# Kernel tuning notes

Measured on AMD Instinct MI355X. Metric: run time of the kernel, lower is better.

Reference implementation:

```python
import jax, jax.numpy as jnp
import numpy as np

DIM = 1024
CROSS_DIM = 768
NUM_HEADS = 16
HEAD_DIM = DIM // NUM_HEADS
B, S, SC = 4, 2048, 1024


def setup_inputs() -> dict:
    key = jax.random.key(0)
    ks = jax.random.split(key, 12)
    x = jax.random.normal(ks[0], (B, S, DIM), dtype=jnp.float32)
    cross_x = jax.random.normal(ks[1], (B, SC, CROSS_DIM), dtype=jnp.float32)
    # ragged cross lengths -> padding mask (True = ignore)
    lengths = jax.random.randint(ks[2], (B,), SC // 2, SC + 1)
    key_padding_mask = jnp.arange(SC)[None, :] >= lengths[:, None]  # (B, SC) bool
    s = 0.02
    Wq = jax.random.normal(ks[3], (DIM, DIM), dtype=jnp.float32) * s
    bq = jnp.zeros((DIM,), dtype=jnp.float32)
    Wk = jax.random.normal(ks[4], (CROSS_DIM, DIM), dtype=jnp.float32) * s
    bk = jnp.zeros((DIM,), dtype=jnp.float32)
    Wv = jax.random.normal(ks[5], (CROSS_DIM, DIM), dtype=jnp.float32) * s
    bv = jnp.zeros((DIM,), dtype=jnp.float32)
    Wo = jax.random.normal(ks[6], (DIM, DIM), dtype=jnp.float32) * s
    bo = jnp.zeros((DIM,), dtype=jnp.float32)
    return {"x": x, "cross_x": cross_x, "key_padding_mask": key_padding_mask,
            "Wq": Wq, "bq": bq, "Wk": Wk, "bk": bk, "Wv": Wv, "bv": bv,
            "Wo": Wo, "bo": bo}


def reference(x, cross_x, key_padding_mask, Wq, bq, Wk, bk, Wv, bv, Wo, bo):
    b, s, _ = x.shape
    sc = cross_x.shape[1]
    # projections (torch Linear: x @ W + b with W stored as (in, out) here)
    q = (x @ Wq + bq).reshape(b, s, NUM_HEADS, HEAD_DIM).transpose(0, 2, 1, 3)
    k = (cross_x @ Wk + bk).reshape(b, sc, NUM_HEADS, HEAD_DIM).transpose(0, 2, 1, 3)
    v = (cross_x @ Wv + bv).reshape(b, sc, NUM_HEADS, HEAD_DIM).transpose(0, 2, 1, 3)
    # (b, h, s, sc) attention scores
    scores = jnp.einsum('bhsd,bhcd->bhsc', q, k) / jnp.sqrt(jnp.float32(HEAD_DIM))
    mask = key_padding_mask[:, None, None, :]  # (b,1,1,sc), True = ignore
    scores = jnp.where(mask, -jnp.inf, scores)
    # original subtracts row max then softmax; equivalent stable softmax
    scores = scores - jnp.max(scores, axis=-1, keepdims=True)
    attn = jax.nn.softmax(scores, axis=-1)
    out = jnp.einsum('bhsc,bhcd->bhsd', attn, v)
    out = out.transpose(0, 2, 1, 3).reshape(b, s, DIM)
    return out @ Wo + bo
```

## Files before the change

### kernel.cpp

```cpp
#include <hip/hip_runtime.h>
#include <hip/hip_bf16.h>
#include <stdint.h>

#define DIM_ 1024
#define NH_ 16
#define HD_ 64
#define B_ 4
#define S_ 2048
#define SC_ 1024
#define CD_ 768

typedef __attribute__((ext_vector_type(8))) short bf16x8;
typedef __attribute__((ext_vector_type(4))) short bf16x4;
typedef __attribute__((ext_vector_type(4))) float f32x4;

__device__ inline unsigned short f2bf(float f) {
    __hip_bfloat16 h = __float2bfloat16(f);
    return __builtin_bit_cast(unsigned short, h);
}

__device__ inline f32x4 vmax4(f32x4 a, f32x4 b) {
    f32x4 r;
#pragma unroll
    for (int i = 0; i < 4; ++i) r[i] = fmaxf(a[i], b[i]);
    return r;
}

#define GLOAD16(SRC, DST) __builtin_amdgcn_global_load_lds( \
    (const __attribute__((address_space(1))) void*)(SRC),   \
    (__attribute__((address_space(3))) void*)(DST), 16, 0, 0)

__global__ void k_f32_to_bf16(const float* __restrict__ in, unsigned short* __restrict__ out, int n4) {
    int i = blockIdx.x * blockDim.x + threadIdx.x;
    int stride = gridDim.x * blockDim.x;
    for (; i < n4; i += stride) {
        float4 v = ((const float4*)in)[i];
        uint2 pk;
        pk.x = (unsigned int)f2bf(v.x) | ((unsigned int)f2bf(v.y) << 16);
        pk.y = (unsigned int)f2bf(v.z) | ((unsigned int)f2bf(v.w) << 16);
        ((uint2*)out)[i] = pk;
    }
}

__global__ void k_transposeW4(const float* __restrict__ Wq, const float* __restrict__ Wk,
                              const float* __restrict__ Wv, const float* __restrict__ Wo,
                              unsigned short* __restrict__ WQT, unsigned short* __restrict__ WKT,
                              unsigned short* __restrict__ WVT, unsigned short* __restrict__ WOT) {
    int idx = blockIdx.x * blockDim.x + threadIdx.x;
    const float* W; unsigned short* WT; int K;
    if (idx < 131072)      { W = Wq; WT = WQT; K = 1024; }
    else if (idx < 229376) { W = Wk; WT = WKT; K = 768;  idx -= 131072; }
    else if (idx < 327680) { W = Wv; WT = WVT; K = 768;  idx -= 229376; }
    else                   { W = Wo; WT = WOT; K = 1024; idx -= 327680; }
    int n = idx & 1023;
    int k0 = (idx >> 10) << 3;
    unsigned int pk[4];
#pragma unroll
    for (int j = 0; j < 4; ++j) {
        unsigned short a = f2bf(W[(size_t)(k0 + 2 * j) * 1024 + n]);
        unsigned short b = f2bf(W[(size_t)(k0 + 2 * j + 1) * 1024 + n]);
        pk[j] = (unsigned int)a | ((unsigned int)b << 16);
    }
    *(uint4*)&WT[(size_t)n * K + k0] = *(uint4*)pk;
}

__global__ void k_mask_bits(const unsigned int* __restrict__ m,
                            unsigned int* __restrict__ bits, int* __restrict__ ntp) {
    __shared__ int bm_s;
    __shared__ unsigned int wbits[128];
    if (threadIdx.x == 0) bm_s = 0;
    __syncthreads();
    int any = 0;
    for (int i = threadIdx.x; i < 1024; i += 256)
        if (m[i] > 1u) any = 1;
    if (any) atomicOr(&bm_s, 1);
    __syncthreads();
    const int boolmode = bm_s;
    const int w = threadIdx.x;
    if (w < 128) {
        const unsigned char* mb = (const unsigned char*)m;
        unsigned int out = 0;
        for (int j = 0; j < 32; ++j) {
            int c = w * 32 + j;
            int masked = boolmode ? (mb[c] != 0) : (m[c] != 0u);
            out |= (unsigned int)masked << j;
        }
        bits[w] = out;
        wbits[w] = out;
    }
    __syncthreads();
    if (threadIdx.x < 4) {
        int nt = 0;
        for (int tt = 0; tt < 16; ++tt) {
            unsigned int w0 = wbits[threadIdx.x * 32 + tt * 2];
            unsigned int w1 = wbits[threadIdx.x * 32 + tt * 2 + 1];
            if ((w0 & w1) != 0xFFFFFFFFu) nt = tt + 1;
        }
        ntp[threadIdx.x] = nt;
    }
}

template<int EPI>
__global__ __launch_bounds__(256) void k_gemm_bt(
    const unsigned short* __restrict__ A, const unsigned short* __restrict__ BT,
    const float* __restrict__ bias, const float* __restrict__ bias2, float oscale,
    unsigned short* __restrict__ Cb, unsigned short* __restrict__ Cb2,
    float* __restrict__ Cf, int M, int N, int K)
{
    __shared__ unsigned short As[2][128 * 32];
    __shared__ unsigned short Bs[2][128 * 32];
    const int t = threadIdx.x;
    const int w = t >> 6, lane = t & 63;
    const int lo = lane & 15, hi = lane >> 4;
    const int nwg = gridDim.x * gridDim.y;
    const int wg = blockIdx.y * gridDim.x + blockIdx.x;
    const int swz = (wg & 7) * (nwg >> 3) + (wg >> 3);
    const int m0 = (swz % gridDim.x) * 128, n0 = (swz / gridDim.x) * 128;
    const int wr = (w >> 1) * 64, wc = (w & 1) * 64;
    const int srow = lane >> 2;
    const int scol = (lane & 3) * 8;

    f32x4 zero4 = {0.f, 0.f, 0.f, 0.f};
    f32x4 acc[4][4];
    for (int i = 0; i < 4; ++i)
        for (int j = 0; j < 4; ++j) acc[i][j] = zero4;

#pragma unroll
    for (int p = 0; p < 2; ++p) {
        int chunk = w * 2 + p;
        int r = chunk * 16 + srow;
        GLOAD16(&A[(size_t)(m0 + r) * K + scol], &As[0][chunk * 512]);
        GLOAD16(&BT[(size_t)(n0 + r) * K + scol], &Bs[0][chunk * 512]);
    }
    __syncthreads();

    int cur = 0;
    for (int k0 = 0; k0 < K; k0 += 32) {
        if (k0 + 32 < K) {
#pragma unroll
            for (int p = 0; p < 2; ++p) {
                int chunk = w * 2 + p;
                int r = chunk * 16 + srow;
                GLOAD16(&A[(size_t)(m0 + r) * K + k0 + 32 + scol], &As[cur ^ 1][chunk * 512]);
                GLOAD16(&BT[(size_t)(n0 + r) * K + k0 + 32 + scol], &Bs[cur ^ 1][chunk * 512]);
            }
        }
        bf16x8 af[4], bfr[4];
#pragma unroll
        for (int i = 0; i < 4; ++i)
            af[i] = *(const bf16x8*)&As[cur][(wr + i * 16 + lo) * 32 + (hi << 3)];
#pragma unroll
        for (int j = 0; j < 4; ++j)
            bfr[j] = *(const bf16x8*)&Bs[cur][(wc + j * 16 + lo) * 32 + (hi << 3)];
#pragma unroll
        for (int i = 0; i < 4; ++i)
#pragma unroll
            for (int j = 0; j < 4; ++j)
                acc[i][j] = __builtin_amdgcn_mfma_f32_16x16x32_bf16(af[i], bfr[j], acc[i][j], 0, 0, 0);
        __syncthreads();
        cur ^= 1;
    }

#pragma unroll
    for (int i = 0; i < 4; ++i) {
#pragma unroll
        for (int j = 0; j < 4; ++j) {
            int n = n0 + wc + j * 16 + lo;
            int mbase = m0 + wr + i * 16 + (hi << 2);
            if (EPI == 3 && n >= 1024) {
                float b2 = bias2[n - 1024];
                uint2 pk;
                pk.x = (unsigned int)f2bf(acc[i][j][0] + b2) | ((unsigned int)f2bf(acc[i][j][1] + b2) << 16);
                pk.y = (unsigned int)f2bf(acc[i][j][2] + b2) | ((unsigned int)f2bf(acc[i][j][3] + b2) << 16);
                int bb = mbase >> 10, c = mbase & 1023;
                *(uint2*)&Cb2[(size_t)((bb << 10) + (n - 1024)) * 1024 + c] = pk;
            } else {
#pragma unroll
                for (int r = 0; r < 4; ++r) {
                    int m = mbase + r;
                    if (EPI == 0) {
                        float v = (acc[i][j][r] + bias[n]) * oscale;
                        Cb[(size_t)m * 1024 + n] = f2bf(v);
                    } else if (EPI == 2) {
                        float v = (acc[i][j][r] + bias[n]) * oscale;
                        Cf[(size_t)m * 1024 + n] = v;
                    } else {
                        float v = acc[i][j][r] + bias[n];
                        Cb[(size_t)m * 1024 + n] = f2bf(v);
                    }
                }
            }
        }
    }
}

__global__ __launch_bounds__(256) void k_attn(
    const unsigned short* __restrict__ Q, const unsigned short* __restrict__ Kb,
    const unsigned short* __restrict__ VT, const unsigned int* __restrict__ bits,
    const int* __restrict__ ntp, unsigned short* __restrict__ Ob)
{
    __shared__ unsigned short lds[16384];
    const int t = threadIdx.x, w = t >> 6, lane = t & 63;
    const int lo = lane & 15, hi = lane >> 4;
    const int qt = blockIdx.x, h = blockIdx.y, b = blockIdx.z;
    const int qr0 = qt * 128 + w * 32;
    const int l7 = lo & 7;
    const int nt = ntp[b];

    const int srow = lane >> 3;
    const int scb  = ((lane & 7) ^ srow) << 3;

    bf16x8 qf[2][2];
#pragma unroll
    for (int qh = 0; qh < 2; ++qh)
#pragma unroll
        for (int kk = 0; kk < 2; ++kk)
            qf[qh][kk] = *(const bf16x8*)&Q[(size_t)(b * S_ + qr0 + qh * 16 + lo) * DIM_ + h * 64 + kk * 32 + hi * 8];

    f32x4 zero4 = {0.f, 0.f, 0.f, 0.f};
    float mrow[2] = {-1e30f, -1e30f}, lsum[2] = {0.f, 0.f};
    f32x4 o[4][2];
#pragma unroll
    for (int dt = 0; dt < 4; ++dt)
#pragma unroll
        for (int qh = 0; qh < 2; ++qh) o[dt][qh] = zero4;

#pragma unroll
    for (int s = 0; s < 2; ++s) {
        int rl = w * 16 + s * 8 + srow;
        GLOAD16(&Kb[(size_t)(b * SC_ + rl) * DIM_ + h * 64 + scb], &lds[(w * 16 + s * 8) * 64]);
        GLOAD16(&VT[(size_t)(b * 1024 + h * 64 + rl) * SC_ + scb], &lds[8192 + (w * 16 + s * 8) * 64]);
    }
    __syncthreads();

    int cur = 0;
    for (int tt = 0; tt < nt; ++tt) {
        if (tt + 1 < nt) {
            int c0n = (tt + 1) * 64;
#pragma unroll
            for (int s = 0; s < 2; ++s) {
                int rl = w * 16 + s * 8 + srow;
                GLOAD16(&Kb[(size_t)(b * SC_ + c0n + rl) * DIM_ + h * 64 + scb],
                        &lds[(cur ^ 1) * 4096 + (w * 16 + s * 8) * 64]);
                GLOAD16(&VT[(size_t)(b * 1024 + h * 64 + rl) * SC_ + c0n + scb],
                        &lds[8192 + (cur ^ 1) * 4096 + (w * 16 + s * 8) * 64]);
            }
        }
        const unsigned short* Kl = &lds[cur * 4096];
        const unsigned short* Vl = &lds[8192 + cur * 4096];

        f32x4 st[4][2];
#pragma unroll
        for (int n = 0; n < 4; ++n)
#pragma unroll
            for (int qh = 0; qh < 2; ++qh) st[n][qh] = zero4;
#pragma unroll
        for (int n = 0; n < 4; ++n) {
            const int R = n * 16 + lo;
            bf16x8 k0 = *(const bf16x8*)&Kl[R * 64 + ((hi ^ l7) << 3)];
            bf16x8 k1 = *(const bf16x8*)&Kl[R * 64 + (((4 + hi) ^ l7) << 3)];
#pragma unroll
            for (int qh = 0; qh < 2; ++qh) {
                st[n][qh] = __builtin_amdgcn_mfma_f32_16x16x32_bf16(k0, qf[qh][0], st[n][qh], 0, 0, 0);
                st[n][qh] = __builtin_amdgcn_mfma_f32_16x16x32_bf16(k1, qf[qh][1], st[n][qh], 0, 0, 0);
            }
        }
        bf16x4 vf[4][4];
#pragma unroll
        for (int dt = 0; dt < 4; ++dt)
#pragma unroll
            for (int n = 0; n < 4; ++n)
                vf[dt][n] = *(const bf16x4*)&Vl[(dt * 16 + lo) * 64
                              + (((2 * n + (hi >> 1)) ^ l7) << 3) + ((hi & 1) << 2)];

        uint2 mw = *(const uint2*)&bits[b * 32 + tt * 2];

        f32x4 p[2][4];
        float mx[2];
        if ((mw.x | mw.y) == 0u) {
#pragma unroll
            for (int qh = 0; qh < 2; ++qh) {
                f32x4 a = vmax4(vmax4(st[0][qh], st[1][qh]), vmax4(st[2][qh], st[3][qh]));
                mx[qh] = fmaxf(fmaxf(a[0], a[1]), fmaxf(a[2], a[3]));
#pragma unroll
                for (int n = 0; n < 4; ++n) p[qh][n] = st[n][qh];
            }
        } else {
            mx[0] = -1e30f; mx[1] = -1e30f;
#pragma unroll
            for (int n = 0; n < 4; ++n) {
                unsigned int wd = (n & 2) ? mw.y : mw.x;
#pragma unroll
                for (int r = 0; r < 4; ++r) {
                    int sh = ((n & 1) << 4) + (hi << 2) + r;
                    bool mk = (wd >> sh) & 1u;
#pragma unroll
                    for (int qh = 0; qh < 2; ++qh) {
                        float s = mk ? -1e30f : st[n][qh][r];
                        p[qh][n][r] = s;
                        mx[qh] = fmaxf(mx[qh], s);
                    }
                }
            }
        }
        float m2[2];
#pragma unroll
        for (int qh = 0; qh < 2; ++qh) {
            float v = fmaxf(mx[qh], __shfl_xor(mx[qh], 16));
            m2[qh] = fmaxf(v, __shfl_xor(v, 32));
        }
        float growth = fmaxf(m2[0] - mrow[0], m2[1] - mrow[1]);
        if (!__all(growth <= 8.0f)) {
#pragma unroll
            for (int qh = 0; qh < 2; ++qh) {
                float mnew = fmaxf(mrow[qh], m2[qh]);
                float scl = __builtin_amdgcn_exp2f(mrow[qh] - mnew);
                mrow[qh] = mnew;
                lsum[qh] *= scl;
#pragma unroll
                for (int dt = 0; dt < 4; ++dt)
                    o[dt][qh] *= scl;
            }
        }
#pragma unroll
        for (int qh = 0; qh < 2; ++qh) {
            f32x4 rs4 = zero4;
#pragma unroll
            for (int n = 0; n < 4; ++n) {
                f32x4 e;
#pragma unroll
                for (int r = 0; r < 4; ++r)
                    e[r] = __builtin_amdgcn_exp2f(p[qh][n][r] - mrow[qh]);
                p[qh][n] = e;
                rs4 += e;
            }
            float rs = (rs4[0] + rs4[1]) + (rs4[2] + rs4[3]);
            rs += __shfl_xor(rs, 16);
            rs += __shfl_xor(rs, 32);
            lsum[qh] += rs;
        }
#pragma unroll
        for (int qh = 0; qh < 2; ++qh) {
#pragma unroll
            for (int n = 0; n < 4; ++n) {
                uint2 pk2;
                pk2.x = (unsigned int)f2bf(p[qh][n][0]) | ((unsigned int)f2bf(p[qh][n][1]) << 16);
                pk2.y = (unsigned int)f2bf(p[qh][n][2]) | ((unsigned int)f2bf(p[qh][n][3]) << 16);
                bf16x4 pb = __builtin_bit_cast(bf16x4, pk2);
#pragma unroll
                for (int dt = 0; dt < 4; ++dt)
                    o[dt][qh] = __builtin_amdgcn_mfma_f32_16x16x16bf16_1k(vf[dt][n], pb, o[dt][qh], 0, 0, 0);
            }
        }
        __syncthreads();
        cur ^= 1;
    }

    unsigned short* Tl = &lds[w * 2304];
    float inv[2] = {1.0f / lsum[0], 1.0f / lsum[1]};
#pragma unroll
    for (int qh = 0; qh < 2; ++qh)
#pragma unroll
        for (int dt = 0; dt < 4; ++dt)
#pragma unroll
            for (int r = 0; r < 4; ++r)
                Tl[(qh * 16 + lo) * 72 + dt * 16 + hi * 4 + r] = f2bf(o[dt][qh][r] * inv[qh]);
#pragma unroll
    for (int ps = 0; ps < 4; ++ps) {
        int row = ps * 8 + (lane >> 3);
        int col = (lane & 7) * 8;
        bf16x8 v = *(const bf16x8*)&Tl[row * 72 + col];
        *(bf16x8*)&Ob[(size_t)(b * S_ + qr0 + row) * DIM_ + h * 64 + col] = v;
    }
}

extern "C" void kernel_launch(void* const* d_in, const int* in_sizes, int n_in,
                              void* d_out, int out_size, void* d_ws, size_t ws_size,
                              hipStream_t stream)
{
    const float* x  = (const float*)d_in[0];
    const float* cx = (const float*)d_in[1];
    const void* mask = d_in[2];
    const float* Wq = (const float*)d_in[3];
    const float* bq = (const float*)d_in[4];
    const float* Wk = (const float*)d_in[5];
    const float* bk = (const float*)d_in[6];
    const float* Wv = (const float*)d_in[7];
    const float* bv = (const float*)d_in[8];
    const float* Wo = (const float*)d_in[9];
    const float* bo = (const float*)d_in[10];

    unsigned short* ws = (unsigned short*)d_ws;
    const size_t XB  = 0;
    const size_t CXB = XB  + (size_t)8192 * 1024;
    const size_t WQT = CXB + (size_t)4096 * 768;
    const size_t WKT = WQT + (size_t)1024 * 1024;
    const size_t WVT = WKT + (size_t)1024 * 768;
    const size_t WOT = WVT + (size_t)1024 * 768;
    const size_t QB  = WOT + (size_t)1024 * 1024;
    const size_t KB  = QB  + (size_t)8192 * 1024;
    const size_t VTB = KB  + (size_t)4096 * 1024;
    const size_t MBT = VTB + (size_t)4 * 1024 * 1024;
    const size_t NTP = MBT + 256;

    k_f32_to_bf16<<<2048, 256, 0, stream>>>(x,  ws + XB,  8192 * 1024 / 4);
    k_f32_to_bf16<<<2048, 256, 0, stream>>>(cx, ws + CXB, 4096 * 768 / 4);
    k_transposeW4<<<1792, 256, 0, stream>>>(Wq, Wk, Wv, Wo, ws + WQT, ws + WKT, ws + WVT, ws + WOT);
    unsigned int* mbits = (unsigned int*)(ws + MBT);
    int* ntp = (int*)(ws + NTP);
    k_mask_bits<<<1, 256, 0, stream>>>((const unsigned int*)mask, mbits, ntp);

    const float QSCALE = 0.125f * 1.44269504088896340736f;
    dim3 gq(8192 / 128, 1024 / 128);
    dim3 gkv(4096 / 128, 2048 / 128);
    k_gemm_bt<0><<<gq, 256, 0, stream>>>(ws + XB, ws + WQT, bq, nullptr, QSCALE, ws + QB, nullptr, nullptr, 8192, 1024, 1024);
    k_gemm_bt<3><<<gkv, 256, 0, stream>>>(ws + CXB, ws + WKT, bk, bv, 1.0f, ws + KB, ws + VTB, nullptr, 4096, 2048, 768);

    dim3 ga(S_ / 128, NH_, B_);
    k_attn<<<ga, 256, 0, stream>>>(ws + QB, ws + KB, ws + VTB, mbits, ntp, ws + XB);

    k_gemm_bt<2><<<gq, 256, 0, stream>>>(ws + XB, ws + WOT, bo, nullptr, 1.0f, nullptr, nullptr, (float*)d_out, 8192, 1024, 1024);
}
```

Measured before the change: 170.7 us.

## Double GEMM K-tile with XOR-swizzled LDS and merge preprocessing launches

The GEMM's K tile grows from 32 to 64, so each main-loop iteration issues twice the MFMAs per barrier. The LDS layout is now XOR-swizzled to avoid bank conflicts on the wider rows. Separately, the two f32-to-bf16 conversion launches are merged into one kernel, and the mask-bit kernel is folded into the weight-transpose launch as an extra block, cutting two kernel launches. LDS use per GEMM block doubles to 64 KB, which may lower occupancy.

```diff
diff --git a/kernel.cpp b/kernel.cpp
--- a/kernel.cpp
+++ b/kernel.cpp
@@ -30,22 +30,62 @@
     (const __attribute__((address_space(1))) void*)(SRC),   \
     (__attribute__((address_space(3))) void*)(DST), 16, 0, 0)
 
-__global__ void k_f32_to_bf16(const float* __restrict__ in, unsigned short* __restrict__ out, int n4) {
+__global__ void k_f32_to_bf16_2(const float* __restrict__ in0, unsigned short* __restrict__ out0, int n40,
+                                const float* __restrict__ in1, unsigned short* __restrict__ out1, int n41) {
     int i = blockIdx.x * blockDim.x + threadIdx.x;
     int stride = gridDim.x * blockDim.x;
-    for (; i < n4; i += stride) {
-        float4 v = ((const float4*)in)[i];
+    int total = n40 + n41;
+    for (; i < total; i += stride) {
+        const float4 v = (i < n40) ? ((const float4*)in0)[i] : ((const float4*)in1)[i - n40];
         uint2 pk;
         pk.x = (unsigned int)f2bf(v.x) | ((unsigned int)f2bf(v.y) << 16);
         pk.y = (unsigned int)f2bf(v.z) | ((unsigned int)f2bf(v.w) << 16);
-        ((uint2*)out)[i] = pk;
+        if (i < n40) ((uint2*)out0)[i] = pk;
+        else         ((uint2*)out1)[i - n40] = pk;
     }
 }
 
 __global__ void k_transposeW4(const float* __restrict__ Wq, const float* __restrict__ Wk,
                               const float* __restrict__ Wv, const float* __restrict__ Wo,
                               unsigned short* __restrict__ WQT, unsigned short* __restrict__ WKT,
-                              unsigned short* __restrict__ WVT, unsigned short* __restrict__ WOT) {
+                              unsigned short* __restrict__ WVT, unsigned short* __restrict__ WOT,
+                              const unsigned int* __restrict__ m,
+                              unsigned int* __restrict__ bits, int* __restrict__ ntp) {
+    if (blockIdx.x == 1792) {
+        __shared__ int bm_s;
+        __shared__ unsigned int wbits[128];
+        if (threadIdx.x == 0) bm_s = 0;
+        __syncthreads();
+        int any = 0;
+        for (int i = threadIdx.x; i < 1024; i += 256)
+            if (m[i] > 1u) any = 1;
+        if (any) atomicOr(&bm_s, 1);
+        __syncthreads();
+        const int boolmode = bm_s;
+        const int w = threadIdx.x;
+        if (w < 128) {
+            const unsigned char* mb = (const unsigned char*)m;
+            unsigned int out = 0;
+            for (int j = 0; j < 32; ++j) {
+                int c = w * 32 + j;
+                int masked = boolmode ? (mb[c] != 0) : (m[c] != 0u);
+                out |= (unsigned int)masked << j;
+            }
+            bits[w] = out;
+            wbits[w] = out;
+        }
+        __syncthreads();
+        if (threadIdx.x < 4) {
+            int nt = 0;
+            for (int tt = 0; tt < 16; ++tt) {
+                unsigned int w0 = wbits[threadIdx.x * 32 + tt * 2];
+                unsigned int w1 = wbits[threadIdx.x * 32 + tt * 2 + 1];
+                if ((w0 & w1) != 0xFFFFFFFFu) nt = tt + 1;
+            }
+            ntp[threadIdx.x] = nt;
+        }
+        return;
+    }
     int idx = blockIdx.x * blockDim.x + threadIdx.x;
     const float* W; unsigned short* WT; int K;
     if (idx < 131072)      { W = Wq; WT = WQT; K = 1024; }
@@ -64,42 +104,6 @@
     *(uint4*)&WT[(size_t)n * K + k0] = *(uint4*)pk;
 }
 
-__global__ void k_mask_bits(const unsigned int* __restrict__ m,
-                            unsigned int* __restrict__ bits, int* __restrict__ ntp) {
-    __shared__ int bm_s;
-    __shared__ unsigned int wbits[128];
-    if (threadIdx.x == 0) bm_s = 0;
-    __syncthreads();
-    int any = 0;
-    for (int i = threadIdx.x; i < 1024; i += 256)
-        if (m[i] > 1u) any = 1;
-    if (any) atomicOr(&bm_s, 1);
-    __syncthreads();
-    const int boolmode = bm_s;
-    const int w = threadIdx.x;
-    if (w < 128) {
-        const unsigned char* mb = (const unsigned char*)m;
-        unsigned int out = 0;
-        for (int j = 0; j < 32; ++j) {
-            int c = w * 32 + j;
-            int masked = boolmode ? (mb[c] != 0) : (m[c] != 0u);
-            out |= (unsigned int)masked << j;
-        }
-        bits[w] = out;
-        wbits[w] = out;
-    }
-    __syncthreads();
-    if (threadIdx.x < 4) {
-        int nt = 0;
-        for (int tt = 0; tt < 16; ++tt) {
-            unsigned int w0 = wbits[threadIdx.x * 32 + tt * 2];
-            unsigned int w1 = wbits[threadIdx.x * 32 + tt * 2 + 1];
-            if ((w0 & w1) != 0xFFFFFFFFu) nt = tt + 1;
-        }
-        ntp[threadIdx.x] = nt;
-    }
-}
-
 template<int EPI>
 __global__ __launch_bounds__(256) void k_gemm_bt(
     const unsigned short* __restrict__ A, const unsigned short* __restrict__ BT,
@@ -107,18 +111,19 @@
     unsigned short* __restrict__ Cb, unsigned short* __restrict__ Cb2,
     float* __restrict__ Cf, int M, int N, int K)
 {
-    __shared__ unsigned short As[2][128 * 32];
-    __shared__ unsigned short Bs[2][128 * 32];
+    __shared__ unsigned short As[2][128 * 64];
+    __shared__ unsigned short Bs[2][128 * 64];
     const int t = threadIdx.x;
     const int w = t >> 6, lane = t & 63;
     const int lo = lane & 15, hi = lane >> 4;
+    const int l7 = lo & 7;
     const int nwg = gridDim.x * gridDim.y;
     const int wg = blockIdx.y * gridDim.x + blockIdx.x;
     const int swz = (wg & 7) * (nwg >> 3) + (wg >> 3);
     const int m0 = (swz % gridDim.x) * 128, n0 = (swz / gridDim.x) * 128;
     const int wr = (w >> 1) * 64, wc = (w & 1) * 64;
-    const int srow = lane >> 2;
-    const int scol = (lane & 3) * 8;
+    const int srow = lane >> 3;
+    const int scb  = ((lane & 7) ^ srow) << 3;
 
     f32x4 zero4 = {0.f, 0.f, 0.f, 0.f};
     f32x4 acc[4][4];
@@ -126,37 +131,42 @@
         for (int j = 0; j < 4; ++j) acc[i][j] = zero4;
 
 #pragma unroll
-    for (int p = 0; p < 2; ++p) {
-        int chunk = w * 2 + p;
-        int r = chunk * 16 + srow;
-        GLOAD16(&A[(size_t)(m0 + r) * K + scol], &As[0][chunk * 512]);
-        GLOAD16(&BT[(size_t)(n0 + r) * K + scol], &Bs[0][chunk * 512]);
+    for (int p = 0; p < 4; ++p) {
+        int rb = w * 32 + p * 8;
+        GLOAD16(&A[(size_t)(m0 + rb + srow) * K + scb], &As[0][rb * 64]);
+        GLOAD16(&BT[(size_t)(n0 + rb + srow) * K + scb], &Bs[0][rb * 64]);
     }
     __syncthreads();
 
     int cur = 0;
-    for (int k0 = 0; k0 < K; k0 += 32) {
-        if (k0 + 32 < K) {
-#pragma unroll
-            for (int p = 0; p < 2; ++p) {
-                int chunk = w * 2 + p;
-                int r = chunk * 16 + srow;
-                GLOAD16(&A[(size_t)(m0 + r) * K + k0 + 32 + scol], &As[cur ^ 1][chunk * 512]);
-                GLOAD16(&BT[(size_t)(n0 + r) * K + k0 + 32 + scol], &Bs[cur ^ 1][chunk * 512]);
-            }
-        }
-        bf16x8 af[4], bfr[4];
-#pragma unroll
-        for (int i = 0; i < 4; ++i)
-            af[i] = *(const bf16x8*)&As[cur][(wr + i * 16 + lo) * 32 + (hi << 3)];
-#pragma unroll
-        for (int j = 0; j < 4; ++j)
-            bfr[j] = *(const bf16x8*)&Bs[cur][(wc + j * 16 + lo) * 32 + (hi << 3)];
-#pragma unroll
-        for (int i = 0; i < 4; ++i)
-#pragma unroll
-            for (int j = 0; j < 4; ++j)
-                acc[i][j] = __builtin_amdgcn_mfma_f32_16x16x32_bf16(af[i], bfr[j], acc[i][j], 0, 0, 0);
+    for (int k0 = 0; k0 < K; k0 += 64) {
+        if (k0 + 64 < K) {
+#pragma unroll
+            for (int p = 0; p < 4; ++p) {
+                int rb = w * 32 + p * 8;
+                GLOAD16(&A[(size_t)(m0 + rb + srow) * K + k0 + 64 + scb], &As[cur ^ 1][rb * 64]);
+                GLOAD16(&BT[(size_t)(n0 + rb + srow) * K + k0 + 64 + scb], &Bs[cur ^ 1][rb * 64]);
+            }
+        }
+#pragma unroll
+        for (int kk = 0; kk < 2; ++kk) {
+            bf16x8 af[4], bfr[4];
+#pragma unroll
+            for (int i = 0; i < 4; ++i) {
+                int row = wr + i * 16 + lo;
+                af[i] = *(const bf16x8*)&As[cur][row * 64 + ((((kk << 2) + hi) ^ l7) << 3)];
+            }
+#pragma unroll
+            for (int j = 0; j < 4; ++j) {
+                int row = wc + j * 16 + lo;
+                bfr[j] = *(const bf16x8*)&Bs[cur][row * 64 + ((((kk << 2) + hi) ^ l7) << 3)];
+            }
+#pragma unroll
+            for (int i = 0; i < 4; ++i)
+#pragma unroll
+                for (int j = 0; j < 4; ++j)
+                    acc[i][j] = __builtin_amdgcn_mfma_f32_16x16x32_bf16(af[i], bfr[j], acc[i][j], 0, 0, 0);
+        }
         __syncthreads();
         cur ^= 1;
     }
@@ -403,12 +413,14 @@
     const size_t MBT = VTB + (size_t)4 * 1024 * 1024;
     const size_t NTP = MBT + 256;
 
-    k_f32_to_bf16<<<2048, 256, 0, stream>>>(x,  ws + XB,  8192 * 1024 / 4);
-    k_f32_to_bf16<<<2048, 256, 0, stream>>>(cx, ws + CXB, 4096 * 768 / 4);
-    k_transposeW4<<<1792, 256, 0, stream>>>(Wq, Wk, Wv, Wo, ws + WQT, ws + WKT, ws + WVT, ws + WOT);
     unsigned int* mbits = (unsigned int*)(ws + MBT);
     int* ntp = (int*)(ws + NTP);
-    k_mask_bits<<<1, 256, 0, stream>>>((const unsigned int*)mask, mbits, ntp);
+
+    k_f32_to_bf16_2<<<2048, 256, 0, stream>>>(x, ws + XB, 8192 * 1024 / 4,
+                                              cx, ws + CXB, 4096 * 768 / 4);
+    k_transposeW4<<<1793, 256, 0, stream>>>(Wq, Wk, Wv, Wo,
+                                            ws + WQT, ws + WKT, ws + WVT, ws + WOT,
+                                            (const unsigned int*)mask, mbits, ntp);
 
     const float QSCALE = 0.125f * 1.44269504088896340736f;
     dim3 gq(8192 / 128, 1024 / 128);
```

Result: faster. 153.8 us (-9.9%).
